# Kernel tuning notes

Measured on AMD Instinct MI355X. Metric: run time of the kernel, lower is better.

The kernel has to match this reference:

```python
import jax, jax.numpy as jnp
import numpy as np

B, T, D = 32, 2048, 80
K1 = K2 = 3
S1 = S2 = 2
CB_DIM, CB_SIZE = 512, 1024
MASK_P = 0.1
NOISE_STD = 0.1
INPUT_DIM = D * K1 * K2  # 720


def _win_idx(T_in, k, s):
    Tp = (T_in - k) // s + 1
    return jnp.arange(Tp)[:, None] * s + jnp.arange(k)[None, :]  # (Tp, k)


def _unfold(x, k, s):
    # matches torch x.unfold(1, k, s).view(B, Tp, -1): out[b, t, f*k + j] = x[b, t*s + j, f]
    idx = _win_idx(x.shape[1], k, s)
    w = x[:, idx, :]                 # (B, Tp, k, F)
    w = jnp.swapaxes(w, 2, 3)        # (B, Tp, F, k)
    return w.reshape(w.shape[0], w.shape[1], -1)


def setup_inputs() -> dict:
    key = jax.random.key(0)
    k1, k2, k3, k4, k5 = jax.random.split(key, 5)
    raw_feats = jax.random.normal(k1, (B, T, D), jnp.float32)
    auged_feats = jax.random.normal(k2, (B, T, D), jnp.float32)
    length = jax.random.randint(k3, (B,), T // 2, T + 1)
    xav = (2.0 / (INPUT_DIM + CB_DIM)) ** 0.5  # xavier_normal std
    projector = jax.random.normal(k4, (INPUT_DIM, CB_DIM), jnp.float32) * xav
    codebook = jax.random.normal(k5, (CB_SIZE, CB_DIM), jnp.float32)
    return {"raw_feats": raw_feats, "auged_feats": auged_feats, "length": length,
            "projector": projector, "codebook": codebook}


def reference(raw_feats, auged_feats, length, projector, codebook):
    T1 = (T - K1) // S1 + 1
    T2 = (T1 - K2) // S2 + 1
    idx1 = _win_idx(T, K1, S1)                         # (T1, K1)
    idx2 = _win_idx(T1, K2, S2)                        # (T2, K2)
    frame_windows = idx1[idx2].reshape(T2, K1 * K2)    # (T2, 9) original frame idx per subsampled step
    label_lengths = ((length - K1) // S1 + 1 - K2) // S2 + 1  # (B,)

    # --- label path: two torch-style unfolds -> project -> nearest codebook entry ---
    stacked = _unfold(_unfold(raw_feats, K1, S1), K2, S2)     # (B, T2, 720)
    targets = jnp.matmul(stacked, projector)                  # (B, T2, 512)
    # squared-euclidean expansion; same argmin as ||t - c||
    dist = (jnp.sum(targets * targets, axis=-1, keepdims=True)
            - 2.0 * jnp.einsum('btd,cd->btc', targets, codebook)
            + jnp.sum(codebook * codebook, axis=-1))          # (B, T2, 1024)
    labels = jnp.argmin(dist, axis=-1) + 1                    # labels start from 1; 0 = ignore idx
    valid = jnp.arange(T2)[None, :] < label_lengths[:, None]  # (B, T2)
    labels = jnp.where(valid, labels, 0)[None]                # (num_codebooks=1, B, T2)

    # --- static (span length 1) random masking on valid subsampled steps ---
    mkey = jax.random.key(42)
    km, kn = jax.random.split(mkey)
    masked = (jax.random.uniform(km, (B, T2)) < MASK_P) & valid
    masked_dim = masked.astype(jnp.float32)                   # (B, T2)
    # scatter masked subsampled steps back onto original frame indices (union of windows)
    hits = jnp.zeros((B, T), jnp.float32).at[:, frame_windows].add(masked_dim[:, :, None])
    frame_mask = hits > 0                                     # (B, T)
    noise = NOISE_STD * jax.random.normal(kn, (B, T, D), auged_feats.dtype)
    masked_feats = jnp.where(frame_mask[:, :, None], noise, auged_feats)
    return masked_feats, labels, masked_dim
```

## Files before the change

kernel.cpp:

```cpp
#include <hip/hip_runtime.h>
#include <cstdint>

#define B_    32
#define T_    2048
#define D_    80
#define T2_   511
#define NROW  16352
#define GK    720
#define CBD   512
#define CBS   1024
#define HMASK 8176
#define HN    2621440
#define NP    16384
#define KB    23

using bfrag = __attribute__((ext_vector_type(8))) short;
using f32x4 = __attribute__((ext_vector_type(4))) float;
using s4    = __attribute__((ext_vector_type(4))) short;

__device__ inline ushort f2bf(float f){
  uint32_t u = __float_as_uint(f);
  uint32_t r = (u + 0x7FFFu + ((u >> 16) & 1u)) >> 16;
  return (ushort)r;
}
__device__ inline float bf2f(ushort h){ return __uint_as_float(((uint32_t)h) << 16); }

#define GLL16(gsrc, ldst) __builtin_amdgcn_global_load_lds( \
    (__attribute__((address_space(1))) void*)(gsrc), \
    (__attribute__((address_space(3))) void*)(ldst), 16, 0, 0)

__host__ __device__ inline uint32_t rotl_(uint32_t v, int d){ return (v<<d)|(v>>(32-d)); }

__host__ __device__ inline void tf2x32(uint32_t k0, uint32_t k1, uint32_t& x0, uint32_t& x1){
  uint32_t ks2 = k0 ^ k1 ^ 0x1BD11BDAu;
  x0 += k0; x1 += k1;
  const int r0[4] = {13,15,26,6}, r1[4] = {17,29,16,24};
#pragma unroll
  for (int i=0;i<4;i++){ x0 += x1; x1 = rotl_(x1, r0[i]); x1 ^= x0; }
  x0 += k1; x1 += ks2 + 1u;
#pragma unroll
  for (int i=0;i<4;i++){ x0 += x1; x1 = rotl_(x1, r1[i]); x1 ^= x0; }
  x0 += ks2; x1 += k0 + 2u;
#pragma unroll
  for (int i=0;i<4;i++){ x0 += x1; x1 = rotl_(x1, r0[i]); x1 ^= x0; }
  x0 += k0; x1 += k1 + 3u;
#pragma unroll
  for (int i=0;i<4;i++){ x0 += x1; x1 = rotl_(x1, r1[i]); x1 ^= x0; }
  x0 += k1; x1 += ks2 + 4u;
#pragma unroll
  for (int i=0;i<4;i++){ x0 += x1; x1 = rotl_(x1, r0[i]); x1 ^= x0; }
  x0 += ks2; x1 += k0 + 5u;
}

__device__ inline float erfinv_f(float x){
  float w = -log1pf(-x*x);
  float p;
  if (w < 5.0f){
    w -= 2.5f;
    p = 2.81022636e-08f;
    p = fmaf(p, w, 3.43273939e-07f);
    p = fmaf(p, w, -3.5233877e-06f);
    p = fmaf(p, w, -4.39150654e-06f);
    p = fmaf(p, w, 0.00021858087f);
    p = fmaf(p, w, -0.00125372503f);
    p = fmaf(p, w, -0.00417768164f);
    p = fmaf(p, w, 0.246640727f);
    p = fmaf(p, w, 1.50140941f);
  } else {
    w = sqrtf(w) - 3.0f;
    p = -0.000200214257f;
    p = fmaf(p, w, 0.000100950558f);
    p = fmaf(p, w, 0.00134934322f);
    p = fmaf(p, w, -0.00367342844f);
    p = fmaf(p, w, 0.00573950773f);
    p = fmaf(p, w, -0.0076224613f);
    p = fmaf(p, w, 0.00943887047f);
    p = fmaf(p, w, 1.00167406f);
    p = fmaf(p, w, 2.83297682f);
  }
  return p * x;
}

__device__ inline int label_len(int L){ return (((L - 3) / 2) - 2) / 2 + 1; }

__global__ void cbnorm_k(const float* __restrict__ cb, ushort* __restrict__ W0, ushort* __restrict__ W1){
  int c = blockIdx.x, lane = threadIdx.x;
  double s = 0.0;
  for (int k = lane; k < CBD; k += 64){ float v = cb[c*CBD + k]; s += (double)v * (double)v; }
#pragma unroll
  for (int off = 32; off; off >>= 1) s += __shfl_down(s, off);
  float nf = (float)s;
  nf = __shfl(nf, 0);
  size_t base = ((size_t)(KB-1)*CBS + c)*32;
  int sw = ((c >> 1) & 3) << 3;
  if (lane == 16){
    float h = -0.5f * nf;
    ushort h0 = f2bf(h); ushort h1 = f2bf(h - bf2f(h0));
    W0[base + (16 ^ sw)] = h0; W1[base + (16 ^ sw)] = h1;
  } else if (lane > 16 && lane < 32){
    W0[base + (lane ^ sw)] = 0; W1[base + (lane ^ sw)] = 0;
  }
}

__global__ void gather_k(const float* __restrict__ raw, ushort* __restrict__ S0, ushort* __restrict__ S1){
  int idx4 = blockIdx.x * 256 + threadIdx.x;
  int kk4 = idx4 & 7;
  int n   = (idx4 >> 3) & (NP - 1);
  int kb  = idx4 >> 17;
  int b = n / T2_, t2 = n - b * T2_;
  s4 o0, o1;
#pragma unroll
  for (int j = 0; j < 4; ++j){
    int k = kb*32 + kk4*4 + j;
    float v = 0.f;
    if (n < NROW){
      if (k < GK){
        int d = k / 9, rem = k - 9*d;
        int k1 = rem / 3, k2 = rem - 3*k1;
        int tm = 4*t2 + 2*k2 + k1;
        v = raw[(b * T_ + tm) * D_ + d];
      } else if (k == GK) v = 1.f;
    }
    ushort h0 = f2bf(v); ushort h1 = f2bf(v - bf2f(h0));
    o0[j] = (short)h0; o1[j] = (short)h1;
  }
  int kk4s = kk4 ^ ((((n >> 1)) & 3) << 1);
  size_t off = ((size_t)kb*NP + n)*32 + kk4s*4;
  *(s4*)&S0[off] = o0;
  *(s4*)&S1[off] = o1;
}

__global__ __launch_bounds__(256) void wgemm_k(const float* __restrict__ P, const float* __restrict__ cb,
                                               float* __restrict__ Wp){
  __shared__ float sP[16][68];
  __shared__ float sC[16][68];
  int r0 = blockIdx.y * 64, c0 = blockIdx.x * 64;
  int kz = blockIdx.z;
  int tid = threadIdx.x, tx = tid & 15, ty = tid >> 4;
  float acc[4][4] = {};
  for (int k0 = kz * 128; k0 < kz * 128 + 128; k0 += 16){
    __syncthreads();
    {
      int r = tid >> 2, kq = tid & 3;
      int rr = r0 + r;
      float4 v = {0.f,0.f,0.f,0.f};
      if (rr < GK) v = *(const float4*)&P[rr * CBD + k0 + kq * 4];
      sP[kq*4+0][r] = v.x; sP[kq*4+1][r] = v.y; sP[kq*4+2][r] = v.z; sP[kq*4+3][r] = v.w;
      float4 w = *(const float4*)&cb[(c0 + r) * CBD + k0 + kq * 4];
      sC[kq*4+0][r] = w.x; sC[kq*4+1][r] = w.y; sC[kq*4+2][r] = w.z; sC[kq*4+3][r] = w.w;
    }
    __syncthreads();
#pragma unroll
    for (int kk = 0; kk < 16; ++kk){
      float4 a = *(const float4*)&sP[kk][ty * 4];
      float4 b = *(const float4*)&sC[kk][tx * 4];
      float av[4] = {a.x,a.y,a.z,a.w}, bv[4] = {b.x,b.y,b.z,b.w};
#pragma unroll
      for (int i = 0; i < 4; ++i)
#pragma unroll
        for (int j = 0; j < 4; ++j) acc[i][j] = fmaf(av[i], bv[j], acc[i][j]);
    }
  }
#pragma unroll
  for (int i = 0; i < 4; ++i){
    int r = r0 + ty * 4 + i;
    if (r < GK){
      float4 o; o.x = acc[i][0]; o.y = acc[i][1]; o.z = acc[i][2]; o.w = acc[i][3];
      *(float4*)&Wp[((size_t)kz * GK + r) * CBS + c0 + tx * 4] = o;
    }
  }
}

__global__ void wreduce_k(const float* __restrict__ Wp, ushort* __restrict__ W0, ushort* __restrict__ W1){
  int idx = blockIdx.x * 256 + threadIdx.x;
  int r = idx >> 10, c = idx & (CBS - 1);
  float v = Wp[(size_t)r * CBS + c]
          + Wp[((size_t)GK + r) * CBS + c]
          + Wp[((size_t)2*GK + r) * CBS + c]
          + Wp[((size_t)3*GK + r) * CBS + c];
  ushort h0 = f2bf(v); ushort h1 = f2bf(v - bf2f(h0));
  size_t o = ((size_t)(r >> 5) * CBS + c) * 32 + ((r & 31) ^ (((c >> 1) & 3) << 3));
  W0[o] = h0; W1[o] = h1;
}

__global__ __launch_bounds__(256) void score_k(const ushort* __restrict__ S0, const ushort* __restrict__ S1,
                                               const ushort* __restrict__ W0, const ushort* __restrict__ W1,
                                               float* __restrict__ pval, int* __restrict__ pidx){
  __shared__ __align__(16) ushort lA[2][2][128*32];
  __shared__ __align__(16) ushort lB[2][2][128*32];
  int tid = threadIdx.x;
  int lane = tid & 63, wid = tid >> 6;
  int wm = wid >> 1, wn = wid & 1;
  int g = lane >> 4, lr = lane & 15;
  int id = blockIdx.x;
  int xcd = id & 7, slot = id >> 3;
  int cidx = slot & 7, ridx = (xcd << 4) | (slot >> 3);
  int n0 = ridx * 128, c0 = cidx * 128;

  const ushort* base;
  size_t stride32;
  if      (wid == 0){ base = S0 + (size_t)n0*32; stride32 = (size_t)NP*32; }
  else if (wid == 1){ base = S1 + (size_t)n0*32; stride32 = (size_t)NP*32; }
  else if (wid == 2){ base = W0 + (size_t)c0*32; stride32 = (size_t)CBS*32; }
  else              { base = W1 + (size_t)c0*32; stride32 = (size_t)CBS*32; }
  ushort* dstA[2] = { &lA[0][wid&1][0], &lA[1][wid&1][0] };
  ushort* dstB[2] = { &lB[0][wid&1][0], &lB[1][wid&1][0] };

  f32x4 acc[4][4] = {};
  {
    const ushort* src = base;
    ushort* dst = (wid < 2) ? dstA[0] : dstB[0];
#pragma unroll
    for (int q = 0; q < 8; ++q) GLL16(src + q*512 + lane*8, dst + q*512);
  }
  __syncthreads();
  int buf = 0;
  for (int kb = 0; kb < KB; ++kb){
    if (kb + 1 < KB){
      const ushort* src = base + (size_t)(kb+1) * stride32;
      ushort* dst = (wid < 2) ? dstA[buf^1] : dstB[buf^1];
#pragma unroll
      for (int q = 0; q < 8; ++q) GLL16(src + q*512 + lane*8, dst + q*512);
    }
    bfrag a[2][4], bfr[2][4];
#pragma unroll
    for (int mt = 0; mt < 4; ++mt){
      int m = wm*64 + mt*16 + lr;
      int sw = (g ^ ((m >> 1) & 3)) * 8;
      a[0][mt] = *(const bfrag*)&lA[buf][0][m*32 + sw];
      a[1][mt] = *(const bfrag*)&lA[buf][1][m*32 + sw];
    }
#pragma unroll
    for (int nt = 0; nt < 4; ++nt){
      int c = wn*64 + nt*16 + lr;
      int sw = (g ^ ((c >> 1) & 3)) * 8;
      bfr[0][nt] = *(const bfrag*)&lB[buf][0][c*32 + sw];
      bfr[1][nt] = *(const bfrag*)&lB[buf][1][c*32 + sw];
    }
#pragma unroll
    for (int mt = 0; mt < 4; ++mt)
#pragma unroll
      for (int nt = 0; nt < 4; ++nt){
        acc[mt][nt] = __builtin_amdgcn_mfma_f32_16x16x32_bf16(a[0][mt], bfr[0][nt], acc[mt][nt], 0,0,0);
        acc[mt][nt] = __builtin_amdgcn_mfma_f32_16x16x32_bf16(a[0][mt], bfr[1][nt], acc[mt][nt], 0,0,0);
        acc[mt][nt] = __builtin_amdgcn_mfma_f32_16x16x32_bf16(a[1][mt], bfr[0][nt], acc[mt][nt], 0,0,0);
      }
    __syncthreads();
    buf ^= 1;
  }
  float bv[4][4]; int bi[4][4];
#pragma unroll
  for (int mt = 0; mt < 4; ++mt)
#pragma unroll
    for (int r = 0; r < 4; ++r){
      float best = 3.4e38f; int besti = 0;
#pragma unroll
      for (int nt = 0; nt < 4; ++nt){
        float d = -2.f * acc[mt][nt][r];
        int c = c0 + wn*64 + nt*16 + lr;
        if (d < best){ best = d; besti = c; }
      }
      bv[mt][r] = best; bi[mt][r] = besti;
    }
#pragma unroll
  for (int off = 1; off < 16; off <<= 1){
#pragma unroll
    for (int mt = 0; mt < 4; ++mt)
#pragma unroll
      for (int r = 0; r < 4; ++r){
        float ov = __shfl_xor(bv[mt][r], off);
        int   oi = __shfl_xor(bi[mt][r], off);
        if (ov < bv[mt][r] || (ov == bv[mt][r] && oi < bi[mt][r])){ bv[mt][r] = ov; bi[mt][r] = oi; }
      }
  }
  if (lr == 0){
    int p = cidx*2 + wn;
#pragma unroll
    for (int mt = 0; mt < 4; ++mt)
#pragma unroll
      for (int r = 0; r < 4; ++r){
        int n = n0 + wm*64 + mt*16 + g*4 + r;
        pval[(size_t)p*NP + n] = bv[mt][r];
        pidx[(size_t)p*NP + n] = bi[mt][r];
      }
  }
}

__global__ void combine_k(const float* __restrict__ pval, const int* __restrict__ pidx,
                          const int* __restrict__ len, float* __restrict__ lb){
  int n = blockIdx.x * 256 + threadIdx.x;
  if (n >= NROW) return;
  float bv = pval[n]; int bi = pidx[n];
#pragma unroll
  for (int p = 1; p < 16; ++p){
    float v = pval[(size_t)p*NP + n]; int ii = pidx[(size_t)p*NP + n];
    if (v < bv || (v == bv && ii < bi)){ bv = v; bi = ii; }
  }
  int b = n / T2_, t2 = n - b * T2_;
  lb[n] = (t2 < label_len(len[b])) ? (float)(bi + 1) : 0.f;
}

__device__ inline void emit_mask(const int* len, float* md, int i, uint32_t bits){
  float u = __uint_as_float((bits >> 9) | 0x3F800000u) - 1.0f;
  int b = i / T2_, t2 = i - b * T2_;
  bool m = (u < 0.1f) && (t2 < label_len(len[b]));
  md[i] = m ? 1.0f : 0.0f;
}

__global__ void mask_k(const int* __restrict__ len, float* __restrict__ md, uint32_t km0, uint32_t km1){
  int j = blockIdx.x * 256 + threadIdx.x;
  if (j >= HMASK) return;
  uint32_t x0 = (uint32_t)j, x1 = (uint32_t)(j + HMASK);
  tf2x32(km0, km1, x0, x1);
  emit_mask(len, md, j, x0);
  emit_mask(len, md, j + HMASK, x1);
}

__device__ inline void emit_feat(const float* aug, const float* md, float* mf, int i, uint32_t bits){
  int tabs = i / D_;
  int t = tabs & (T_ - 1);
  int b = i / (D_ * T_);
  int lo = (t < 3) ? 0 : ((t - 3) >> 2);
  int hi = t >> 2; if (hi > T2_ - 1) hi = T2_ - 1;
  bool m = false;
  for (int t2 = lo; t2 <= hi; ++t2) m = m || (md[b * T2_ + t2] != 0.f);
  float v;
  if (m){
    float f = __uint_as_float((bits >> 9) | 0x3F800000u) - 1.0f;
    const float LOV = -0.99999994f;
    float u = fmaf(f, 2.0f, LOV);
    u = fmaxf(LOV, u);
    v = 0.1f * (1.41421356f * erfinv_f(u));
  } else {
    v = aug[i];
  }
  mf[i] = v;
}

__global__ void feats_k(const float* __restrict__ aug, const float* __restrict__ md,
                        float* __restrict__ mf, uint32_t kn0, uint32_t kn1){
  int j = blockIdx.x * 256 + threadIdx.x;
  uint32_t x0 = (uint32_t)j, x1 = (uint32_t)(j + HN);
  tf2x32(kn0, kn1, x0, x1);
  emit_feat(aug, md, mf, j, x0);
  emit_feat(aug, md, mf, j + HN, x1);
}

extern "C" void kernel_launch(void* const* d_in, const int* in_sizes, int n_in,
                              void* d_out, int out_size, void* d_ws, size_t ws_size,
                              hipStream_t stream){
  const float* raw  = (const float*)d_in[0];
  const float* aug  = (const float*)d_in[1];
  const int*   len  = (const int*)  d_in[2];
  const float* proj = (const float*)d_in[3];
  const float* cb   = (const float*)d_in[4];

  float* out = (float*)d_out;
  float* mf  = out;
  float* lb  = out + 5242880;
  float* md  = out + 5259232;

  ushort* w  = (ushort*)d_ws;
  ushort* W0 = w;
  ushort* W1 = W0 + (size_t)KB*CBS*32;
  ushort* S0 = W1 + (size_t)KB*CBS*32;
  ushort* S1 = S0 + (size_t)KB*NP*32;
  float* pval = (float*)(S1 + (size_t)KB*NP*32);
  int*   pidx = (int*)(pval + (size_t)16*NP);
  float* Wp   = (float*)(pidx + (size_t)16*NP);

  uint32_t a0 = 0u, a1 = 2u, b0 = 1u, b1 = 3u;
  tf2x32(0u, 42u, a0, a1);
  tf2x32(0u, 42u, b0, b1);
  uint32_t km0 = a0, km1 = b0, kn0 = a1, kn1 = b1;

  cbnorm_k<<<CBS, 64, 0, stream>>>(cb, W0, W1);
  wgemm_k<<<dim3(CBS / 64, 12, 4), 256, 0, stream>>>(proj, cb, Wp);
  wreduce_k<<<(GK * CBS) / 256, 256, 0, stream>>>(Wp, W0, W1);
  gather_k<<<(KB * NP * 8) / 256, 256, 0, stream>>>(raw, S0, S1);
  score_k<<<1024, 256, 0, stream>>>(S0, S1, W0, W1, pval, pidx);
  combine_k<<<(NROW + 255) / 256, 256, 0, stream>>>(pval, pidx, len, lb);
  mask_k<<<(HMASK + 255) / 256, 256, 0, stream>>>(len, md, km0, km1);
  feats_k<<<HN / 256, 256, 0, stream>>>(aug, md, mf, kn0, kn1);
}
```

Baseline: 161.0 us.

## Enlarge score GEMM tiles to 256x256 with dynamic LDS and manual waitcnt pipelining

The score kernel tile grows from 128x128 to 256x256 per block, each wave computing 128x128 with 64 accumulators. It uses 128KB of dynamic LDS with explicit vmcnt waits and raw barriers in place of __syncthreads. The grid drops from 1024 to 256 blocks, and combine reduces over 8 partials instead of 16. gather_k now writes 8-element vectors per thread. The intent is more data reuse per LDS load and fewer partial outputs, at the cost of heavy register pressure (256 accumulator floats) and only 256 blocks, which may underfill the CUs.

```diff
diff --git a/kernel.cpp b/kernel.cpp
--- a/kernel.cpp
+++ b/kernel.cpp
@@ -17,6 +17,7 @@
 using bfrag = __attribute__((ext_vector_type(8))) short;
 using f32x4 = __attribute__((ext_vector_type(4))) float;
 using s4    = __attribute__((ext_vector_type(4))) short;
+using s8    = __attribute__((ext_vector_type(8))) short;
 
 __device__ inline ushort f2bf(float f){
   uint32_t u = __float_as_uint(f);
@@ -103,15 +104,15 @@
 }
 
 __global__ void gather_k(const float* __restrict__ raw, ushort* __restrict__ S0, ushort* __restrict__ S1){
-  int idx4 = blockIdx.x * 256 + threadIdx.x;
-  int kk4 = idx4 & 7;
-  int n   = (idx4 >> 3) & (NP - 1);
-  int kb  = idx4 >> 17;
+  int idx = blockIdx.x * 256 + threadIdx.x;
+  int g  = idx & 3;
+  int n  = (idx >> 2) & (NP - 1);
+  int kb = idx >> 16;
   int b = n / T2_, t2 = n - b * T2_;
-  s4 o0, o1;
-#pragma unroll
-  for (int j = 0; j < 4; ++j){
-    int k = kb*32 + kk4*4 + j;
+  s8 o0, o1;
+#pragma unroll
+  for (int j = 0; j < 8; ++j){
+    int k = kb*32 + g*8 + j;
     float v = 0.f;
     if (n < NROW){
       if (k < GK){
@@ -124,10 +125,10 @@
     ushort h0 = f2bf(v); ushort h1 = f2bf(v - bf2f(h0));
     o0[j] = (short)h0; o1[j] = (short)h1;
   }
-  int kk4s = kk4 ^ ((((n >> 1)) & 3) << 1);
-  size_t off = ((size_t)kb*NP + n)*32 + kk4s*4;
-  *(s4*)&S0[off] = o0;
-  *(s4*)&S1[off] = o1;
+  int gs = g ^ ((n >> 1) & 3);
+  size_t off = ((size_t)kb*NP + n)*32 + gs*8;
+  *(s8*)&S0[off] = o0;
+  *(s8*)&S1[off] = o1;
 }
 
 __global__ __launch_bounds__(256) void wgemm_k(const float* __restrict__ P, const float* __restrict__ cb,
@@ -183,106 +184,112 @@
   W0[o] = h0; W1[o] = h1;
 }
 
-__global__ __launch_bounds__(256) void score_k(const ushort* __restrict__ S0, const ushort* __restrict__ S1,
-                                               const ushort* __restrict__ W0, const ushort* __restrict__ W1,
-                                               float* __restrict__ pval, int* __restrict__ pidx){
-  __shared__ __align__(16) ushort lA[2][2][128*32];
-  __shared__ __align__(16) ushort lB[2][2][128*32];
+__global__ __launch_bounds__(256, 1) void score_k(const ushort* __restrict__ S0, const ushort* __restrict__ S1,
+                                                  const ushort* __restrict__ W0, const ushort* __restrict__ W1,
+                                                  float* __restrict__ pval, int* __restrict__ pidx){
+  extern __shared__ ushort lds[];
   int tid = threadIdx.x;
   int lane = tid & 63, wid = tid >> 6;
   int wm = wid >> 1, wn = wid & 1;
   int g = lane >> 4, lr = lane & 15;
+  int gsw = g ^ ((lr >> 1) & 3);
+
   int id = blockIdx.x;
   int xcd = id & 7, slot = id >> 3;
-  int cidx = slot & 7, ridx = (xcd << 4) | (slot >> 3);
-  int n0 = ridx * 128, c0 = cidx * 128;
-
-  const ushort* base;
-  size_t stride32;
-  if      (wid == 0){ base = S0 + (size_t)n0*32; stride32 = (size_t)NP*32; }
-  else if (wid == 1){ base = S1 + (size_t)n0*32; stride32 = (size_t)NP*32; }
-  else if (wid == 2){ base = W0 + (size_t)c0*32; stride32 = (size_t)CBS*32; }
-  else              { base = W1 + (size_t)c0*32; stride32 = (size_t)CBS*32; }
-  ushort* dstA[2] = { &lA[0][wid&1][0], &lA[1][wid&1][0] };
-  ushort* dstB[2] = { &lB[0][wid&1][0], &lB[1][wid&1][0] };
-
-  f32x4 acc[4][4] = {};
+  int cidx = slot & 3, ridx = (xcd << 3) | (slot >> 2);
+  int n0 = ridx * 256, c0 = cidx * 256;
+
+  const ushort* src0;
+  size_t kstride;
+  if      (wid == 0){ src0 = S0 + (size_t)n0*32; kstride = (size_t)NP*32; }
+  else if (wid == 1){ src0 = S1 + (size_t)n0*32; kstride = (size_t)NP*32; }
+  else if (wid == 2){ src0 = W0 + (size_t)c0*32; kstride = (size_t)CBS*32; }
+  else              { src0 = W1 + (size_t)c0*32; kstride = (size_t)CBS*32; }
+
+  f32x4 acc[8][8] = {};
+
   {
-    const ushort* src = base;
-    ushort* dst = (wid < 2) ? dstA[0] : dstB[0];
-#pragma unroll
-    for (int q = 0; q < 8; ++q) GLL16(src + q*512 + lane*8, dst + q*512);
-  }
-  __syncthreads();
+    ushort* dst = lds + (size_t)wid*8192;
+#pragma unroll
+    for (int q = 0; q < 16; ++q) GLL16(src0 + q*512 + lane*8, dst + q*512);
+  }
   int buf = 0;
   for (int kb = 0; kb < KB; ++kb){
     if (kb + 1 < KB){
-      const ushort* src = base + (size_t)(kb+1) * stride32;
-      ushort* dst = (wid < 2) ? dstA[buf^1] : dstB[buf^1];
-#pragma unroll
-      for (int q = 0; q < 8; ++q) GLL16(src + q*512 + lane*8, dst + q*512);
-    }
-    bfrag a[2][4], bfr[2][4];
-#pragma unroll
-    for (int mt = 0; mt < 4; ++mt){
-      int m = wm*64 + mt*16 + lr;
-      int sw = (g ^ ((m >> 1) & 3)) * 8;
-      a[0][mt] = *(const bfrag*)&lA[buf][0][m*32 + sw];
-      a[1][mt] = *(const bfrag*)&lA[buf][1][m*32 + sw];
-    }
-#pragma unroll
-    for (int nt = 0; nt < 4; ++nt){
-      int c = wn*64 + nt*16 + lr;
-      int sw = (g ^ ((c >> 1) & 3)) * 8;
-      bfr[0][nt] = *(const bfrag*)&lB[buf][0][c*32 + sw];
-      bfr[1][nt] = *(const bfrag*)&lB[buf][1][c*32 + sw];
-    }
-#pragma unroll
-    for (int mt = 0; mt < 4; ++mt)
-#pragma unroll
-      for (int nt = 0; nt < 4; ++nt){
-        acc[mt][nt] = __builtin_amdgcn_mfma_f32_16x16x32_bf16(a[0][mt], bfr[0][nt], acc[mt][nt], 0,0,0);
-        acc[mt][nt] = __builtin_amdgcn_mfma_f32_16x16x32_bf16(a[0][mt], bfr[1][nt], acc[mt][nt], 0,0,0);
-        acc[mt][nt] = __builtin_amdgcn_mfma_f32_16x16x32_bf16(a[1][mt], bfr[0][nt], acc[mt][nt], 0,0,0);
+      const ushort* s = src0 + (size_t)(kb+1)*kstride;
+      ushort* dst = lds + (size_t)((buf^1)*4 + wid)*8192;
+#pragma unroll
+      for (int q = 0; q < 16; ++q) GLL16(s + q*512 + lane*8, dst + q*512);
+      asm volatile("s_waitcnt vmcnt(16)" ::: "memory");
+    } else {
+      asm volatile("s_waitcnt vmcnt(0)" ::: "memory");
+    }
+    __builtin_amdgcn_s_barrier();
+    __builtin_amdgcn_sched_barrier(0);
+
+    const ushort* A0 = lds + (size_t)(buf*4 + 0)*8192;
+    const ushort* A1 = lds + (size_t)(buf*4 + 1)*8192;
+    const ushort* B0 = lds + (size_t)(buf*4 + 2)*8192;
+    const ushort* B1 = lds + (size_t)(buf*4 + 3)*8192;
+
+    bfrag a0[8], a1[8], b0[8], b1[8];
+#pragma unroll
+    for (int mt = 0; mt < 8; ++mt){
+      int off = (wm*128 + mt*16 + lr)*32 + gsw*8;
+      a0[mt] = *(const bfrag*)&A0[off];
+      a1[mt] = *(const bfrag*)&A1[off];
+    }
+#pragma unroll
+    for (int nt = 0; nt < 8; ++nt){
+      int off = (wn*128 + nt*16 + lr)*32 + gsw*8;
+      b0[nt] = *(const bfrag*)&B0[off];
+      b1[nt] = *(const bfrag*)&B1[off];
+    }
+#pragma unroll
+    for (int mt = 0; mt < 8; ++mt)
+#pragma unroll
+      for (int nt = 0; nt < 8; ++nt){
+        acc[mt][nt] = __builtin_amdgcn_mfma_f32_16x16x32_bf16(a0[mt], b0[nt], acc[mt][nt], 0,0,0);
+        acc[mt][nt] = __builtin_amdgcn_mfma_f32_16x16x32_bf16(a0[mt], b1[nt], acc[mt][nt], 0,0,0);
+        acc[mt][nt] = __builtin_amdgcn_mfma_f32_16x16x32_bf16(a1[mt], b0[nt], acc[mt][nt], 0,0,0);
       }
-    __syncthreads();
+    __builtin_amdgcn_sched_barrier(0);
+    __builtin_amdgcn_s_barrier();
     buf ^= 1;
   }
-  float bv[4][4]; int bi[4][4];
-#pragma unroll
-  for (int mt = 0; mt < 4; ++mt)
+
+#pragma unroll
+  for (int mt = 0; mt < 8; ++mt){
+    float bv[4]; int bi[4];
 #pragma unroll
     for (int r = 0; r < 4; ++r){
       float best = 3.4e38f; int besti = 0;
 #pragma unroll
-      for (int nt = 0; nt < 4; ++nt){
+      for (int nt = 0; nt < 8; ++nt){
         float d = -2.f * acc[mt][nt][r];
-        int c = c0 + wn*64 + nt*16 + lr;
+        int c = c0 + wn*128 + nt*16 + lr;
         if (d < best){ best = d; besti = c; }
       }
-      bv[mt][r] = best; bi[mt][r] = besti;
-    }
-#pragma unroll
-  for (int off = 1; off < 16; off <<= 1){
-#pragma unroll
-    for (int mt = 0; mt < 4; ++mt)
+      bv[r] = best; bi[r] = besti;
+    }
+#pragma unroll
+    for (int off = 1; off < 16; off <<= 1){
 #pragma unroll
       for (int r = 0; r < 4; ++r){
-        float ov = __shfl_xor(bv[mt][r], off);
-        int   oi = __shfl_xor(bi[mt][r], off);
-        if (ov < bv[mt][r] || (ov == bv[mt][r] && oi < bi[mt][r])){ bv[mt][r] = ov; bi[mt][r] = oi; }
+        float ov = __shfl_xor(bv[r], off);
+        int   oi = __shfl_xor(bi[r], off);
+        if (ov < bv[r] || (ov == bv[r] && oi < bi[r])){ bv[r] = ov; bi[r] = oi; }
       }
-  }
-  if (lr == 0){
-    int p = cidx*2 + wn;
-#pragma unroll
-    for (int mt = 0; mt < 4; ++mt)
+    }
+    if (lr == 0){
+      int p = cidx*2 + wn;
 #pragma unroll
       for (int r = 0; r < 4; ++r){
-        int n = n0 + wm*64 + mt*16 + g*4 + r;
-        pval[(size_t)p*NP + n] = bv[mt][r];
-        pidx[(size_t)p*NP + n] = bi[mt][r];
+        int n = n0 + wm*128 + mt*16 + g*4 + r;
+        pval[(size_t)p*NP + n] = bv[r];
+        pidx[(size_t)p*NP + n] = bi[r];
       }
+    }
   }
 }
 
@@ -292,7 +299,7 @@
   if (n >= NROW) return;
   float bv = pval[n]; int bi = pidx[n];
 #pragma unroll
-  for (int p = 1; p < 16; ++p){
+  for (int p = 1; p < 8; ++p){
     float v = pval[(size_t)p*NP + n]; int ii = pidx[(size_t)p*NP + n];
     if (v < bv || (v == bv && ii < bi)){ bv = v; bi = ii; }
   }
@@ -369,6 +376,8 @@
   int*   pidx = (int*)(pval + (size_t)16*NP);
   float* Wp   = (float*)(pidx + (size_t)16*NP);
 
+  hipFuncSetAttribute((const void*)score_k, hipFuncAttributeMaxDynamicSharedMemorySize, 131072);
+
   uint32_t a0 = 0u, a1 = 2u, b0 = 1u, b1 = 3u;
   tf2x32(0u, 42u, a0, a1);
   tf2x32(0u, 42u, b0, b1);
@@ -377,8 +386,8 @@
   cbnorm_k<<<CBS, 64, 0, stream>>>(cb, W0, W1);
   wgemm_k<<<dim3(CBS / 64, 12, 4), 256, 0, stream>>>(proj, cb, Wp);
   wreduce_k<<<(GK * CBS) / 256, 256, 0, stream>>>(Wp, W0, W1);
-  gather_k<<<(KB * NP * 8) / 256, 256, 0, stream>>>(raw, S0, S1);
-  score_k<<<1024, 256, 0, stream>>>(S0, S1, W0, W1, pval, pidx);
+  gather_k<<<(KB * NP * 4) / 256, 256, 0, stream>>>(raw, S0, S1);
+  score_k<<<256, 256, 131072, stream>>>(S0, S1, W0, W1, pval, pidx);
   combine_k<<<(NROW + 255) / 256, 256, 0, stream>>>(pval, pidx, len, lb);
   mask_k<<<(HMASK + 255) / 256, 256, 0, stream>>>(len, md, km0, km1);
   feats_k<<<HN / 256, 256, 0, stream>>>(aug, md, mf, kn0, kn1);
```

Result: faster. 151.7 us (-5.8%).
